# Kernel tuning notes

Measured on AMD Instinct MI355X. Metric: run time of the kernel, lower is better.

Reference implementation:

```python
import jax, jax.numpy as jnp
import numpy as np
import math

B, S, D = 2, 2048, 1024
H = 16
HD = D // H
FFN = 2048
E = 8
TOP_K = 2
CAP_FACTOR = 1.25
EPS = 1e-6
BASE = 10000.0
CAP = max(math.ceil(B * S * TOP_K * CAP_FACTOR / E), 1)  # 1280


def setup_inputs() -> dict:
    key = jax.random.key(0)
    ks = jax.random.split(key, 6)
    sd = 0.02
    return {
        "x": jax.random.normal(ks[0], (B, S, D), jnp.float32),
        "g1": jnp.ones((D,), jnp.float32),
        "w_qkv": jax.random.normal(ks[1], (D, 3 * D), jnp.float32) * sd,
        "w_o": jax.random.normal(ks[2], (D, D), jnp.float32) * sd,
        "g2": jnp.ones((D,), jnp.float32),
        "w_router": jax.random.normal(ks[3], (D, E), jnp.float32) * sd,
        "w1": jax.random.normal(ks[4], (E, D, FFN), jnp.float32) * sd,
        "w2": jax.random.normal(ks[5], (E, FFN, D), jnp.float32) * sd,
    }


def _rmsnorm(x, w):
    rms = jax.lax.rsqrt(jnp.mean(x * x, axis=-1, keepdims=True) + EPS)
    return w * x * rms


def _rope(x, cos, sin):
    # x: [b,h,s,hd]; consecutive pairs (2i, 2i+1) form complex numbers
    xr = x[..., 0::2]
    xi = x[..., 1::2]
    c = cos[None, None]  # [1,1,s,hd/2]
    s_ = sin[None, None]
    out_r = xr * c - xi * s_
    out_i = xr * s_ + xi * c
    return jnp.stack([out_r, out_i], axis=-1).reshape(x.shape)


def _mha(x, w_qkv, w_o):
    b, s, d = x.shape
    qkv = x @ w_qkv
    q, k, v = jnp.split(qkv, 3, axis=-1)
    to_heads = lambda z: z.reshape(b, s, H, HD).transpose(0, 2, 1, 3)
    q, k, v = to_heads(q), to_heads(k), to_heads(v)
    # rotary embedding
    theta = BASE ** (-2.0 * (jnp.arange(HD // 2, dtype=jnp.float32) / HD))
    freqs = jnp.arange(s, dtype=jnp.float32)[:, None] * theta[None, :]  # [s,hd/2]
    cos, sin = jnp.cos(freqs), jnp.sin(freqs)
    q = _rope(q, cos, sin)
    k = _rope(k, cos, sin)
    scores = jnp.einsum('bhqd,bhkd->bhqk', q, k) / jnp.sqrt(jnp.float32(HD))
    causal = jnp.tril(jnp.ones((s, s), dtype=bool))
    scores = jnp.where(causal, scores, -jnp.inf)
    attn = jax.nn.softmax(scores, axis=-1)
    y = jnp.einsum('bhqk,bhkd->bhqd', attn, v)
    y = y.transpose(0, 2, 1, 3).reshape(b, s, d)
    return y @ w_o


def _moe(x, w_router, w1, w2):
    b, s, d = x.shape
    t = b * s
    xf = x.reshape(t, d)
    logits = xf.astype(jnp.float32) @ w_router.astype(jnp.float32)
    probs = jax.nn.softmax(logits, axis=-1)  # [t,E]
    g, eidx = jax.lax.top_k(probs, TOP_K)  # [t,K]
    fg = g.reshape(t * TOP_K)
    fe = eidx.reshape(t * TOP_K)
    tok_of = jnp.arange(t * TOP_K) // TOP_K
    # per-expert masked gates, then capacity-based top-CAP selection
    masked = jnp.where(fe[None, :] == jnp.arange(E)[:, None], fg[None, :], -jnp.inf)  # [E, t*K]
    vals, idx = jax.lax.top_k(masked, CAP)  # [E, CAP]
    valid = jnp.isfinite(vals)
    gates = jnp.where(valid, vals, 0.0)  # dropped/empty slots get zero gate
    tok = tok_of[idx]  # [E, CAP] token ids (arbitrary for invalid slots, gate 0)
    xe = xf[tok]  # [E, CAP, d]
    h = jax.nn.relu(jnp.einsum('ecd,edf->ecf', xe, w1))
    ye = jnp.einsum('ecf,efd->ecd', h, w2) * gates[..., None]
    y = jnp.zeros_like(xf).at[tok.reshape(-1)].add(ye.reshape(-1, d))
    return y.reshape(b, s, d)


def reference(x, g1, w_qkv, w_o, g2, w_router, w1, w2):
    x = x + _mha(_rmsnorm(x, g1), w_qkv, w_o)
    x = x + _moe(_rmsnorm(x, g2), w_router, w1, w2)
    return x
```

## Files before the change

kernel.cpp:

```cpp
#include <hip/hip_runtime.h>
#include <math.h>


#define B_   2
#define S_   2048
#define D_   1024
#define H_   16
#define HD_  64
#define FFN_ 2048
#define E_   8
#define CAP_ 1280
#define T_   (B_*S_)

typedef unsigned short u16;
typedef __attribute__((ext_vector_type(8))) short     short8;
typedef __attribute__((ext_vector_type(8))) _Float16  half8;
typedef __attribute__((ext_vector_type(4))) _Float16  half4;
typedef __attribute__((ext_vector_type(8))) unsigned short ushort8v;
typedef __attribute__((ext_vector_type(4))) float     f32x4;

__device__ __forceinline__ u16 f2bf(float f) {
  unsigned u = __float_as_uint(f);
  return (u16)((u + 0x7fffu + ((u >> 16) & 1u)) >> 16);
}
__device__ __forceinline__ float bf2f(u16 h) {
  return __uint_as_float(((unsigned)h) << 16);
}
__device__ __forceinline__ u16 f2h(float f) {
  _Float16 h = (_Float16)f;
  return __builtin_bit_cast(u16, h);
}
__device__ __forceinline__ float h2f(u16 b) {
  return (float)__builtin_bit_cast(_Float16, b);
}

__device__ __forceinline__ void cstore(float* p, float v) { *p = v; }
__device__ __forceinline__ void cstore(u16* p, float v)   { *p = f2bf(v); }

__device__ __forceinline__ void glds16(const u16* g, u16* l) {
  __builtin_amdgcn_global_load_lds(
      (const __attribute__((address_space(1))) unsigned int*)g,
      (__attribute__((address_space(3))) unsigned int*)l, 16, 0, 0);
}

__global__ void init_k(int* cnt) {
  if (threadIdx.x < 16) cnt[threadIdx.x] = 0;
}

__global__ __launch_bounds__(256) void rmsnorm_k(const float* __restrict__ x,
                                                 const float* __restrict__ g,
                                                 float* __restrict__ of,
                                                 u16*   __restrict__ ob,
                                                 u16*   __restrict__ ohh,
                                                 u16*   __restrict__ ohl) {
  const int t = blockIdx.x, tid = threadIdx.x;
  const float4 xv = ((const float4*)(x + (size_t)t * D_))[tid];
  float ss = xv.x*xv.x + xv.y*xv.y + xv.z*xv.z + xv.w*xv.w;
  #pragma unroll
  for (int off = 32; off; off >>= 1) ss += __shfl_down(ss, off);
  __shared__ float wsum[4];
  if ((tid & 63) == 0) wsum[tid >> 6] = ss;
  __syncthreads();
  const float tot = wsum[0] + wsum[1] + wsum[2] + wsum[3];
  const float rms = 1.0f / sqrtf(tot * (1.0f / D_) + 1e-6f);
  const float4 gv = ((const float4*)g)[tid];
  float4 o;
  o.x = gv.x * xv.x * rms;
  o.y = gv.y * xv.y * rms;
  o.z = gv.z * xv.z * rms;
  o.w = gv.w * xv.w * rms;
  if (of) ((float4*)(of + (size_t)t * D_))[tid] = o;
  if (ob) {
    ushort4 h;
    h.x = f2bf(o.x); h.y = f2bf(o.y); h.z = f2bf(o.z); h.w = f2bf(o.w);
    ((ushort4*)(ob + (size_t)t * D_))[tid] = h;
  }
  if (ohh) {
    ushort4 hh, hl;
    hh.x = f2h(o.x); hl.x = f2h(o.x - h2f(hh.x));
    hh.y = f2h(o.y); hl.y = f2h(o.y - h2f(hh.y));
    hh.z = f2h(o.z); hl.z = f2h(o.z - h2f(hh.z));
    hh.w = f2h(o.w); hl.w = f2h(o.w - h2f(hh.w));
    ((ushort4*)(ohh + (size_t)t * D_))[tid] = hh;
    ((ushort4*)(ohl + (size_t)t * D_))[tid] = hl;
  }
}

template<bool RESID>
__global__ __launch_bounds__(256) void gemm_split(const u16* __restrict__ Ah,
                                                  const u16* __restrict__ Al,
                                                  const u16* __restrict__ Bh,
                                                  const u16* __restrict__ Bl,
                                                  const float* __restrict__ resid,
                                                  float* __restrict__ C,
                                                  int K, int lda, int ldb, int ldc) {
  __shared__ u16 AsH[128 * 32], AsL[128 * 32];
  __shared__ u16 BsH[128 * 32], BsL[128 * 32];
  const int tid = threadIdx.x;
  const int bm = blockIdx.y, bn = blockIdx.x;
  const int lane = tid & 63, wave = tid >> 6;
  const int wy = wave >> 1, wx = wave & 1;
  const int l15 = lane & 15, lq = lane >> 4;
  f32x4 acc[4][4];
  #pragma unroll
  for (int i = 0; i < 4; ++i)
    #pragma unroll
    for (int j = 0; j < 4; ++j)
      #pragma unroll
      for (int r = 0; r < 4; ++r) acc[i][j][r] = 0.0f;
  const int srow = lane >> 2, skc = (lane & 3) * 8;
  size_t ga[2], gb[2];
  int ldsoff[2];
  #pragma unroll
  for (int c = 0; c < 2; ++c) {
    const int q = wave * 2 + c;
    ga[c] = (size_t)(bm * 128 + q * 16 + srow) * lda + skc;
    gb[c] = (size_t)(bn * 128 + q * 16 + srow) * ldb + skc;
    ldsoff[c] = q * 512 + lane * 8;
  }

  for (int kt = 0; kt < K; kt += 32) {
    __syncthreads();
    #pragma unroll
    for (int c = 0; c < 2; ++c) {
      glds16(Ah + ga[c] + kt, &AsH[ldsoff[c]]);
      glds16(Al + ga[c] + kt, &AsL[ldsoff[c]]);
      glds16(Bh + gb[c] + kt, &BsH[ldsoff[c]]);
      glds16(Bl + gb[c] + kt, &BsL[ldsoff[c]]);
    }
    __syncthreads();
    half8 ah[4], al[4], bh[4], bl[4];
    #pragma unroll
    for (int i = 0; i < 4; ++i) {
      const int row = (wy * 64 + i * 16 + l15) * 32 + lq * 8;
      ah[i] = *(const half8*)&AsH[row];
      al[i] = *(const half8*)&AsL[row];
    }
    #pragma unroll
    for (int j = 0; j < 4; ++j) {
      const int row = (wx * 64 + j * 16 + l15) * 32 + lq * 8;
      bh[j] = *(const half8*)&BsH[row];
      bl[j] = *(const half8*)&BsL[row];
    }
    #pragma unroll
    for (int i = 0; i < 4; ++i)
      #pragma unroll
      for (int j = 0; j < 4; ++j) {
        acc[i][j] = __builtin_amdgcn_mfma_f32_16x16x32_f16(ah[i], bh[j], acc[i][j], 0, 0, 0);
        acc[i][j] = __builtin_amdgcn_mfma_f32_16x16x32_f16(ah[i], bl[j], acc[i][j], 0, 0, 0);
        acc[i][j] = __builtin_amdgcn_mfma_f32_16x16x32_f16(al[i], bh[j], acc[i][j], 0, 0, 0);
      }
  }
  #pragma unroll
  for (int i = 0; i < 4; ++i)
    #pragma unroll
    for (int j = 0; j < 4; ++j)
      #pragma unroll
      for (int r = 0; r < 4; ++r) {
        const int row = bm * 128 + wy * 64 + i * 16 + lq * 4 + r;
        const int col = bn * 128 + wx * 64 + j * 16 + l15;
        float v = acc[i][j][r];
        if (RESID) v += resid[(size_t)row * ldc + col];
        C[(size_t)row * ldc + col] = v;
      }
}

__global__ __launch_bounds__(256) void wsplit_t_k(const float* __restrict__ src,
                                                  u16* __restrict__ dh,
                                                  u16* __restrict__ dl,
                                                  int R, int C) {
  __shared__ float tile[32][33];
  const int tid = threadIdx.x;
  const int r0 = blockIdx.y * 32, c0 = blockIdx.x * 32;
  const int tx = tid & 31, ty = tid >> 5;
  #pragma unroll
  for (int i = 0; i < 4; ++i)
    tile[ty + i * 8][tx] = src[(size_t)(r0 + ty + i * 8) * C + c0 + tx];
  __syncthreads();
  #pragma unroll
  for (int i = 0; i < 4; ++i) {
    const float v = tile[tx][ty + i * 8];
    const u16 hh = f2h(v);
    const size_t o = (size_t)(c0 + ty + i * 8) * R + r0 + tx;
    dh[o] = hh;
    dl[o] = f2h(v - h2f(hh));
  }
}

__global__ __launch_bounds__(256) void ropesplit_k(const float* __restrict__ qkv,
                                                   u16* __restrict__ qhi, u16* __restrict__ qlo,
                                                   u16* __restrict__ khi, u16* __restrict__ klo) {
  const int i = blockIdx.x * 256 + threadIdx.x;
  const int j = i & 31;
  const int h = (i >> 5) & 15;
  const int t = i >> 9;
  const int s = t & (S_ - 1);
  const int b = t >> 11;
  const int bh = b * 16 + h;
  const float theta = (float)pow(10000.0, -(double)j / 32.0);
  const float fr = (float)s * theta;
  const float c = cosf(fr), sn = sinf(fr);
  const float2 q = *(const float2*)(qkv + (size_t)t * 3072 + h * 64 + 2 * j);
  const float2 k = *(const float2*)(qkv + (size_t)t * 3072 + 1024 + h * 64 + 2 * j);
  const float q0 = (q.x * c - q.y * sn) * 0.125f;
  const float q1 = (q.x * sn + q.y * c) * 0.125f;
  const float k0 = k.x * c - k.y * sn;
  const float k1 = k.x * sn + k.y * c;
  const size_t o = ((size_t)bh * S_ + s) * 32 + j;
  const u16 qh0 = f2bf(q0), qh1 = f2bf(q1);
  const u16 kh0 = f2bf(k0), kh1 = f2bf(k1);
  ((unsigned*)qhi)[o] = (unsigned)qh0 | ((unsigned)qh1 << 16);
  ((unsigned*)khi)[o] = (unsigned)kh0 | ((unsigned)kh1 << 16);
  const u16 ql0 = f2bf(q0 - bf2f(qh0)), ql1 = f2bf(q1 - bf2f(qh1));
  const u16 kl0 = f2bf(k0 - bf2f(kh0)), kl1 = f2bf(k1 - bf2f(kh1));
  ((unsigned*)qlo)[o] = (unsigned)ql0 | ((unsigned)ql1 << 16);
  ((unsigned*)klo)[o] = (unsigned)kl0 | ((unsigned)kl1 << 16);
}

__global__ __launch_bounds__(256) void vpack_k(const float* __restrict__ qkv,
                                               u16* __restrict__ vpk) {
  const int kt = blockIdx.x, bh = blockIdx.y;
  const int b = bh >> 4, h = bh & 15;
  const int tid = threadIdx.x;
  u16* dst = vpk + (size_t)(bh * 32 + kt) * 8192;
  #pragma unroll
  for (int i = 0; i < 4; ++i) {
    const int g = i * 256 + tid;
    const int lane = g & 63, n = (g >> 6) & 3, kc = g >> 8;
    const int lq = lane >> 4, l15 = lane & 15;
    const int key = kt * 64 + kc * 16 + lq * 4;
    const int d = n * 16 + l15;
    u16 out[8];
    #pragma unroll
    for (int j = 0; j < 4; ++j) {
      const float v = qkv[(size_t)(b * S_ + key + j) * 3072 + 2048 + h * 64 + d];
      const u16 hh = f2h(v);
      out[j] = hh;
      out[4 + j] = f2h(v - h2f(hh));
    }
    *(ushort8v*)(dst + g * 8) = *(ushort8v*)out;
  }
}

__global__ __launch_bounds__(256, 4) void attn_mfma_k(const u16* __restrict__ qhi,
                                                      const u16* __restrict__ qlo,
                                                      const u16* __restrict__ khi,
                                                      const u16* __restrict__ klo,
                                                      const u16* __restrict__ vpk,
                                                      u16* __restrict__ ahh,
                                                      u16* __restrict__ ahl,
                                                      float* __restrict__ PO,
                                                      float* __restrict__ Pm,
                                                      float* __restrict__ Pl2) {
  __shared__ u16 Kh[64 * 68], Kl[64 * 68];
  __shared__ u16 Vp[8192];
  const int tid = threadIdx.x, lane = tid & 63, wave = tid >> 6;
  const int bi = blockIdx.x;
  int qt, k0, k1, chunk;
  bool partial;
  if (bi < 32) {
    qt = 31 - (bi >> 1); chunk = bi & 1;
    const int nk = qt + 1, cut = nk >> 1;
    k0 = chunk ? cut : 0;
    k1 = chunk ? nk : cut;
    partial = true;
  } else {
    qt = 47 - bi; chunk = 0; k0 = 0; k1 = qt + 1; partial = false;
  }
  const int bh = blockIdx.y;
  const int l15 = lane & 15, lq = lane >> 4;
  const size_t hb = (size_t)bh * S_ * 64;
  const int qrow = qt * 64 + wave * 16 + l15;
  short8 qh[2], ql[2];
  qh[0] = *(const short8*)(qhi + hb + (size_t)qrow * 64 + lq * 8);
  qh[1] = *(const short8*)(qhi + hb + (size_t)qrow * 64 + 32 + lq * 8);
  ql[0] = *(const short8*)(qlo + hb + (size_t)qrow * 64 + lq * 8);
  ql[1] = *(const short8*)(qlo + hb + (size_t)qrow * 64 + 32 + lq * 8);
  f32x4 O[4];
  #pragma unroll
  for (int n = 0; n < 4; ++n)
    #pragma unroll
    for (int r = 0; r < 4; ++r) O[n][r] = 0.0f;
  float m_i = -__builtin_inff(), l_i = 0.0f;

  const int sidx0 = tid,       srow0 = sidx0 >> 3, sc80 = (sidx0 & 7) * 8;
  const int sidx1 = 256 + tid, srow1 = sidx1 >> 3, sc81 = (sidx1 & 7) * 8;
  const int vlds = wave * 2048 + lane * 8;
  ushort8v kregH[2], kregL[2], vreg[4];

  auto issue_loads = [&](int kt) {
    const size_t koff0 = hb + (size_t)(kt * 64 + srow0) * 64 + sc80;
    const size_t koff1 = hb + (size_t)(kt * 64 + srow1) * 64 + sc81;
    kregH[0] = *(const ushort8v*)(khi + koff0);
    kregL[0] = *(const ushort8v*)(klo + koff0);
    kregH[1] = *(const ushort8v*)(khi + koff1);
    kregL[1] = *(const ushort8v*)(klo + koff1);
    const u16* vg = vpk + (size_t)(bh * 32 + kt) * 8192 + vlds;
    #pragma unroll
    for (int c = 0; c < 4; ++c)
      vreg[c] = *(const ushort8v*)(vg + c * 512);
  };
  auto write_lds = [&]() {
    *(ushort8v*)&Kh[srow0 * 68 + sc80] = kregH[0];
    *(ushort8v*)&Kl[srow0 * 68 + sc80] = kregL[0];
    *(ushort8v*)&Kh[srow1 * 68 + sc81] = kregH[1];
    *(ushort8v*)&Kl[srow1 * 68 + sc81] = kregL[1];
    #pragma unroll
    for (int c = 0; c < 4; ++c)
      *(ushort8v*)&Vp[vlds + c * 512] = vreg[c];
  };

  issue_loads(k0);
  write_lds();
  __syncthreads();

  for (int kt = k0; kt < k1; ++kt) {
    const bool pf = (kt + 1 < k1);
    if (pf) issue_loads(kt + 1);
    f32x4 sc[4];
    #pragma unroll
    for (int kc = 0; kc < 4; ++kc)
      #pragma unroll
      for (int r = 0; r < 4; ++r) sc[kc][r] = 0.0f;
    __builtin_amdgcn_s_setprio(1);
    #pragma unroll
    for (int kc = 0; kc < 4; ++kc) {
      const int krow = (kc * 16 + l15) * 68 + lq * 8;
      const short8 kb0 = *(const short8*)&Kh[krow];
      const short8 kb1 = *(const short8*)&Kh[krow + 32];
      const short8 kl0 = *(const short8*)&Kl[krow];
      const short8 kl1 = *(const short8*)&Kl[krow + 32];
      sc[kc] = __builtin_amdgcn_mfma_f32_16x16x32_bf16(kb0, qh[0], sc[kc], 0, 0, 0);
      sc[kc] = __builtin_amdgcn_mfma_f32_16x16x32_bf16(kb1, qh[1], sc[kc], 0, 0, 0);
      sc[kc] = __builtin_amdgcn_mfma_f32_16x16x32_bf16(kb0, ql[0], sc[kc], 0, 0, 0);
      sc[kc] = __builtin_amdgcn_mfma_f32_16x16x32_bf16(kb1, ql[1], sc[kc], 0, 0, 0);
      sc[kc] = __builtin_amdgcn_mfma_f32_16x16x32_bf16(kl0, qh[0], sc[kc], 0, 0, 0);
      sc[kc] = __builtin_amdgcn_mfma_f32_16x16x32_bf16(kl1, qh[1], sc[kc], 0, 0, 0);
    }
    __builtin_amdgcn_s_setprio(0);
    if (kt == qt) {
      #pragma unroll
      for (int kc = 0; kc < 4; ++kc)
        #pragma unroll
        for (int r = 0; r < 4; ++r)
          if (kc * 16 + lq * 4 + r > wave * 16 + l15) sc[kc][r] = -__builtin_inff();
    }
    float mx = -__builtin_inff();
    #pragma unroll
    for (int kc = 0; kc < 4; ++kc)
      #pragma unroll
      for (int r = 0; r < 4; ++r) mx = fmaxf(mx, sc[kc][r]);
    mx = fmaxf(mx, __shfl_xor(mx, 16));
    mx = fmaxf(mx, __shfl_xor(mx, 32));
    const float mn = fmaxf(m_i, mx);
    const float alpha = __expf(m_i - mn);
    m_i = mn;
    f32x4 p[4];
    float rs = 0.0f;
    #pragma unroll
    for (int kc = 0; kc < 4; ++kc)
      #pragma unroll
      for (int r = 0; r < 4; ++r) { p[kc][r] = __expf(sc[kc][r] - m_i); rs += p[kc][r]; }
    rs += __shfl_xor(rs, 16);
    rs += __shfl_xor(rs, 32);
    l_i = l_i * alpha + rs;
    #pragma unroll
    for (int r = 0; r < 4; ++r) {
      const float alr = __shfl(alpha, lq * 4 + r);
      #pragma unroll
      for (int n = 0; n < 4; ++n) O[n][r] *= alr;
    }
    half4 ph[4], pl[4];
    #pragma unroll
    for (int kc = 0; kc < 4; ++kc)
      #pragma unroll
      for (int r = 0; r < 4; ++r) {
        const _Float16 hi = (_Float16)p[kc][r];
        ph[kc][r] = hi;
        pl[kc][r] = (_Float16)(p[kc][r] - (float)hi);
      }
    __builtin_amdgcn_s_setprio(1);
    #pragma unroll
    for (int n = 0; n < 4; ++n)
      #pragma unroll
      for (int kc = 0; kc < 4; ++kc) {
        const int g = ((kc * 4 + n) * 64 + lane) * 8;
        const half4 vh = *(const half4*)&Vp[g];
        const half4 vl = *(const half4*)&Vp[g + 4];
        O[n] = __builtin_amdgcn_mfma_f32_16x16x16f16(ph[kc], vh, O[n], 0, 0, 0);
        O[n] = __builtin_amdgcn_mfma_f32_16x16x16f16(ph[kc], vl, O[n], 0, 0, 0);
        O[n] = __builtin_amdgcn_mfma_f32_16x16x16f16(pl[kc], vh, O[n], 0, 0, 0);
      }
    __builtin_amdgcn_s_setprio(0);
    __syncthreads();
    if (pf) write_lds();
    __syncthreads();
  }
  const int b = bh >> 4, h = bh & 15;
  if (!partial) {
    #pragma unroll
    for (int r = 0; r < 4; ++r) {
      const float lr = __shfl(l_i, lq * 4 + r);
      const float inv = 1.0f / lr;
      const int row = qt * 64 + wave * 16 + lq * 4 + r;
      const size_t base = (size_t)(b * S_ + row) * D_ + h * 64 + l15;
      #pragma unroll
      for (int n = 0; n < 4; ++n) {
        const float o = O[n][r] * inv;
        const u16 hh = f2h(o);
        ahh[base + n * 16] = hh;
        ahl[base + n * 16] = f2h(o - h2f(hh));
      }
    }
  } else {
    #pragma unroll
    for (int r = 0; r < 4; ++r) {
      const int prow = qt * 64 + wave * 16 + lq * 4 + r - 1024;
      const size_t idx = (size_t)(chunk * 32 + bh) * 1024 + prow;
      float* po = PO + idx * 64;
      #pragma unroll
      for (int n = 0; n < 4; ++n) po[n * 16 + l15] = O[n][r];
    }
    if (lq == 0) {
      const int prow = qt * 64 + wave * 16 + l15 - 1024;
      const size_t idx = (size_t)(chunk * 32 + bh) * 1024 + prow;
      Pm[idx] = m_i; Pl2[idx] = l_i;
    }
  }
}

__global__ __launch_bounds__(256) void attn_combine_k(const float* __restrict__ PO,
                                                      const float* __restrict__ Pm,
                                                      const float* __restrict__ Pl2,
                                                      u16* __restrict__ ahh,
                                                      u16* __restrict__ ahl) {
  const int tid = threadIdx.x;
  const int bh = blockIdx.y, b = bh >> 4, h = bh & 15;
  const int prow = blockIdx.x * 64 + (tid >> 2);
  const int d0 = (tid & 3) * 16;
  const size_t i0 = (size_t)bh * 1024 + prow;
  const size_t i1 = (size_t)(32 + bh) * 1024 + prow;
  const float m0 = Pm[i0], m1 = Pm[i1];
  const float M = fmaxf(m0, m1);
  const float w0 = __expf(m0 - M), w1 = __expf(m1 - M);
  const float inv = 1.0f / (w0 * Pl2[i0] + w1 * Pl2[i1]);
  const int row = 1024 + prow;
  const size_t ob = (size_t)(b * S_ + row) * D_ + h * 64 + d0;
  #pragma unroll
  for (int q4 = 0; q4 < 4; ++q4) {
    const float4 o0 = *(const float4*)(PO + i0 * 64 + d0 + q4 * 4);
    const float4 o1 = *(const float4*)(PO + i1 * 64 + d0 + q4 * 4);
    float v[4];
    v[0] = (w0 * o0.x + w1 * o1.x) * inv;
    v[1] = (w0 * o0.y + w1 * o1.y) * inv;
    v[2] = (w0 * o0.z + w1 * o1.z) * inv;
    v[3] = (w0 * o0.w + w1 * o1.w) * inv;
    ushort4 hh, hl;
    u16* ph = (u16*)&hh;
    u16* pl = (u16*)&hl;
    #pragma unroll
    for (int z = 0; z < 4; ++z) {
      ph[z] = f2h(v[z]);
      pl[z] = f2h(v[z] - h2f(ph[z]));
    }
    *(ushort4*)(ahh + ob + q4 * 4) = hh;
    *(ushort4*)(ahl + ob + q4 * 4) = hl;
  }
}

__global__ __launch_bounds__(256) void router_k(const float* __restrict__ y2,
                                                const float* __restrict__ wr,
                                                int*   __restrict__ cnt,
                                                int*   __restrict__ tok_e,
                                                float* __restrict__ tok_g,
                                                int*   __restrict__ tok_p,
                                                int*   __restrict__ etok) {
  const int wave = threadIdx.x >> 6, lane = threadIdx.x & 63;
  const int t = blockIdx.x * 4 + wave;
  const float* xr = y2 + (size_t)t * D_;
  float acc[8];
  #pragma unroll
  for (int e = 0; e < 8; ++e) acc[e] = 0.0f;
  for (int c = 0; c < 16; ++c) {
    const float xv = xr[c * 64 + lane];
    const float* w = wr + (size_t)(c * 64 + lane) * 8;
    #pragma unroll
    for (int e = 0; e < 8; ++e) acc[e] = fmaf(xv, w[e], acc[e]);
  }
  #pragma unroll
  for (int off = 32; off; off >>= 1)
    #pragma unroll
    for (int e = 0; e < 8; ++e) acc[e] += __shfl_down(acc[e], off);
  if (lane == 0) {
    float mx = acc[0];
    #pragma unroll
    for (int e = 1; e < 8; ++e) mx = fmaxf(mx, acc[e]);
    float ex[8], sum = 0.0f;
    #pragma unroll
    for (int e = 0; e < 8; ++e) { ex[e] = expf(acc[e] - mx); sum += ex[e]; }
    int e1 = 0;
    #pragma unroll
    for (int e = 1; e < 8; ++e) if (acc[e] > acc[e1]) e1 = e;
    int e2 = (e1 == 0) ? 1 : 0;
    #pragma unroll
    for (int e = 0; e < 8; ++e) if (e != e1 && acc[e] > acc[e2]) e2 = e;
    const float g1v = ex[e1] / sum, g2v = ex[e2] / sum;
    int p1 = atomicAdd(&cnt[e1], 1);
    int p2 = atomicAdd(&cnt[e2], 1);
    if (p1 < CAP_) etok[e1 * CAP_ + p1] = t; else p1 = -1;
    if (p2 < CAP_) etok[e2 * CAP_ + p2] = t; else p2 = -1;
    tok_e[2*t] = e1;   tok_e[2*t+1] = e2;
    tok_g[2*t] = g1v;  tok_g[2*t+1] = g2v;
    tok_p[2*t] = p1;   tok_p[2*t+1] = p2;
  }
}

__global__ __launch_bounds__(256) void gather_k(const u16* __restrict__ y2b,
                                                const int* __restrict__ etok,
                                                const int* __restrict__ cnt,
                                                u16* __restrict__ xe) {
  const int e = blockIdx.y, pos = blockIdx.x, tid = threadIdx.x;
  const int n = min(cnt[e], CAP_);
  ushort4* dst = (ushort4*)(xe + (size_t)(e * CAP_ + pos) * D_) + tid;
  if (pos < n) {
    const int t = etok[e * CAP_ + pos];
    *dst = ((const ushort4*)(y2b + (size_t)t * D_))[tid];
  } else {
    *dst = make_ushort4(0, 0, 0, 0);
  }
}

template<typename OT, bool RELU>
__global__ __launch_bounds__(256) void gemm_bt(const u16* __restrict__ A,
                                               const u16* __restrict__ Bt,
                                               OT* __restrict__ C,
                                               int M, int N, int K,
                                               int lda, int ldb, int ldc,
                                               long sAz, long sBz, long sCz) {
  __shared__ u16 As[128 * 32];
  __shared__ u16 Bs[128 * 32];
  const int tid = threadIdx.x;
  A  += (size_t)blockIdx.z * sAz;
  Bt += (size_t)blockIdx.z * sBz;
  C  += (size_t)blockIdx.z * sCz;
  const int bm = blockIdx.y, bn = blockIdx.x;
  const int lane = tid & 63, wave = tid >> 6;
  const int wy = wave >> 1, wx = wave & 1;
  const int l15 = lane & 15, lq = lane >> 4;
  f32x4 acc[4][4];
  #pragma unroll
  for (int i = 0; i < 4; ++i)
    #pragma unroll
    for (int j = 0; j < 4; ++j)
      #pragma unroll
      for (int r = 0; r < 4; ++r) acc[i][j][r] = 0.0f;
  const int srow = lane >> 2, skc = (lane & 3) * 8;
  size_t ga[2], gb[2];
  int ldsoff[2];
  #pragma unroll
  for (int c = 0; c < 2; ++c) {
    const int q = wave * 2 + c;
    ga[c] = (size_t)(bm * 128 + q * 16 + srow) * lda + skc;
    gb[c] = (size_t)(bn * 128 + q * 16 + srow) * ldb + skc;
    ldsoff[c] = q * 512 + lane * 8;
  }

  for (int kt = 0; kt < K; kt += 32) {
    __syncthreads();
    #pragma unroll
    for (int c = 0; c < 2; ++c) {
      glds16(A  + ga[c] + kt, &As[ldsoff[c]]);
      glds16(Bt + gb[c] + kt, &Bs[ldsoff[c]]);
    }
    __syncthreads();
    short8 a[4], b[4];
    #pragma unroll
    for (int i = 0; i < 4; ++i)
      a[i] = *(const short8*)&As[(wy * 64 + i * 16 + l15) * 32 + lq * 8];
    #pragma unroll
    for (int j = 0; j < 4; ++j)
      b[j] = *(const short8*)&Bs[(wx * 64 + j * 16 + l15) * 32 + lq * 8];
    #pragma unroll
    for (int i = 0; i < 4; ++i)
      #pragma unroll
      for (int j = 0; j < 4; ++j)
        acc[i][j] = __builtin_amdgcn_mfma_f32_16x16x32_bf16(a[i], b[j], acc[i][j], 0, 0, 0);
  }
  #pragma unroll
  for (int i = 0; i < 4; ++i)
    #pragma unroll
    for (int j = 0; j < 4; ++j)
      #pragma unroll
      for (int r = 0; r < 4; ++r) {
        const int row = bm * 128 + wy * 64 + i * 16 + lq * 4 + r;
        const int col = bn * 128 + wx * 64 + j * 16 + l15;
        float v = acc[i][j][r];
        if (RELU) v = fmaxf(v, 0.0f);
        cstore(C + (size_t)row * ldc + col, v);
      }
}

__global__ __launch_bounds__(256) void transpose_bf_k(const float* __restrict__ src,
                                                      u16* __restrict__ dst,
                                                      int R, int C) {
  __shared__ float tile[32][33];
  const int tid = threadIdx.x;
  const size_t zoff = (size_t)blockIdx.z * R * C;
  const int r0 = blockIdx.y * 32, c0 = blockIdx.x * 32;
  const int tx = tid & 31, ty = tid >> 5;
  #pragma unroll
  for (int i = 0; i < 4; ++i)
    tile[ty + i * 8][tx] = src[zoff + (size_t)(r0 + ty + i * 8) * C + c0 + tx];
  __syncthreads();
  #pragma unroll
  for (int i = 0; i < 4; ++i)
    dst[zoff + (size_t)(c0 + ty + i * 8) * R + r0 + tx] = f2bf(tile[tx][ty + i * 8]);
}

__global__ __launch_bounds__(256) void combine_k(const float* __restrict__ x2,
                                                 const float* __restrict__ ye,
                                                 const int*   __restrict__ tok_e,
                                                 const float* __restrict__ tok_g,
                                                 const int*   __restrict__ tok_p,
                                                 float* __restrict__ out) {
  const int t = blockIdx.x, tid = threadIdx.x;
  float4 v = ((const float4*)(x2 + (size_t)t * D_))[tid];
  #pragma unroll
  for (int r = 0; r < 2; ++r) {
    const int p = tok_p[2 * t + r];
    if (p >= 0) {
      const int e = tok_e[2 * t + r];
      const float g = tok_g[2 * t + r];
      const float4 y = ((const float4*)(ye + (size_t)(e * CAP_ + p) * D_))[tid];
      v.x = fmaf(g, y.x, v.x);
      v.y = fmaf(g, y.y, v.y);
      v.z = fmaf(g, y.z, v.z);
      v.w = fmaf(g, y.w, v.w);
    }
  }
  ((float4*)(out + (size_t)t * D_))[tid] = v;
}

extern "C" void kernel_launch(void* const* d_in, const int* in_sizes, int n_in,
                              void* d_out, int out_size, void* d_ws, size_t ws_size,
                              hipStream_t stream) {
  const float* x    = (const float*)d_in[0];
  const float* g1   = (const float*)d_in[1];
  const float* wqkv = (const float*)d_in[2];
  const float* wo   = (const float*)d_in[3];
  const float* g2   = (const float*)d_in[4];
  const float* wr   = (const float*)d_in[5];
  const float* w1   = (const float*)d_in[6];
  const float* w2   = (const float*)d_in[7];
  float* out = (float*)d_out;
  char* ws = (char*)d_ws;
  const size_t MB = 1ull << 20;

  u16*   y1hh  = (u16*)  (ws + 0);
  u16*   y1hl  = (u16*)  (ws + 8 * MB);
  u16*   ahh   = (u16*)  (ws + 16 * MB);
  u16*   ahl   = (u16*)  (ws + 24 * MB);
  u16*   hbf   = (u16*)  (ws + 0);
  float* qkv   = (float*)(ws + 40 * MB);
  float* PO    = (float*)(ws + 40 * MB);
  float* Pm    = (float*)(ws + 58 * MB);
  float* Pl2   = (float*)(ws + 59 * MB);
  u16*   xe    = (u16*)  (ws + 40 * MB);
  float* x2    = (float*)(ws + 88 * MB);
  float* y2    = (float*)(ws + 104 * MB);
  u16*   y2b   = (u16*)  (ws + 120 * MB);
  u16*   w1t   = (u16*)  (ws + 128 * MB);
  u16*   w2t   = (u16*)  (ws + 160 * MB);
  float* ye    = (float*)(ws + 192 * MB);
  u16*   wqh   = (u16*)  (ws + 192 * MB);
  u16*   wql   = (u16*)  (ws + 198 * MB);
  u16*   khi   = (u16*)  (ws + 192 * MB);
  u16*   klo   = (u16*)  (ws + 200 * MB);
  u16*   vpk   = (u16*)  (ws + 208 * MB);
  u16*   woh   = (u16*)  (ws + 224 * MB);
  u16*   wol   = (u16*)  (ws + 226 * MB);
  int*   cnt   = (int*)  (ws + 232 * MB);
  int*   tok_e = cnt + 16;
  float* tok_g = (float*)(tok_e + 2 * T_);
  int*   tok_p = (int*)  (tok_g + 2 * T_);
  int*   etok  = tok_p + 2 * T_;

  init_k<<<1, 64, 0, stream>>>(cnt);
  transpose_bf_k<<<dim3(FFN_/32, D_/32, E_), 256, 0, stream>>>(w1, w1t, D_, FFN_);
  transpose_bf_k<<<dim3(D_/32, FFN_/32, E_), 256, 0, stream>>>(w2, w2t, FFN_, D_);
  wsplit_t_k<<<dim3(3*D_/32, D_/32), 256, 0, stream>>>(wqkv, wqh, wql, D_, 3*D_);
  wsplit_t_k<<<dim3(D_/32, D_/32), 256, 0, stream>>>(wo, woh, wol, D_, D_);

  rmsnorm_k<<<T_, 256, 0, stream>>>(x, g1, (float*)nullptr, (u16*)nullptr, y1hh, y1hl);
  gemm_split<false><<<dim3(3 * D_ / 128, T_ / 128), 256, 0, stream>>>(
      y1hh, y1hl, wqh, wql, nullptr, qkv, D_, D_, D_, 3 * D_);
  ropesplit_k<<<T_ * H_ * 32 / 256, 256, 0, stream>>>(qkv, y1hh, y1hl, khi, klo);
  vpack_k<<<dim3(S_ / 64, B_ * H_), 256, 0, stream>>>(qkv, vpk);
  attn_mfma_k<<<dim3(48, B_ * H_), 256, 0, stream>>>(
      y1hh, y1hl, khi, klo, vpk, ahh, ahl, PO, Pm, Pl2);
  attn_combine_k<<<dim3(16, B_ * H_), 256, 0, stream>>>(PO, Pm, Pl2, ahh, ahl);
  gemm_split<true><<<dim3(D_ / 128, T_ / 128), 256, 0, stream>>>(
      ahh, ahl, woh, wol, x, x2, D_, D_, D_, D_);
  rmsnorm_k<<<T_, 256, 0, stream>>>(x2, g2, y2, y2b, (u16*)nullptr, (u16*)nullptr);
  router_k<<<T_ / 4, 256, 0, stream>>>(y2, wr, cnt, tok_e, tok_g, tok_p, etok);
  gather_k<<<dim3(CAP_, E_), 256, 0, stream>>>(y2b, etok, cnt, xe);
  gemm_bt<u16, true><<<dim3(FFN_/128, CAP_/128, E_), 256, 0, stream>>>(
      xe, w1t, hbf, CAP_, FFN_, D_, D_, D_, FFN_,
      (long)CAP_ * D_, (long)FFN_ * D_, (long)CAP_ * FFN_);
  gemm_bt<float, false><<<dim3(D_/128, CAP_/128, E_), 256, 0, stream>>>(
      hbf, w2t, ye, CAP_, D_, FFN_, FFN_, FFN_, D_,
      (long)CAP_ * FFN_, (long)D_ * FFN_, (long)CAP_ * D_);
  combine_k<<<T_, 256, 0, stream>>>(x2, ye, tok_e, tok_g, tok_p, out);
}
```

Measured before the change: 745.1 us.

## Split attention KV into 8-tile chunks, swizzle K LDS, double-buffer MoE GEMM

Causal attention work is now split into fixed chunks of 8 key tiles, giving 80 blocks per head instead of 48 for finer load balance. Partial results are stored in 72 slots per head, and the combine kernel merges 2 to 4 partials per query tile. The K tiles in LDS move from padded rows to an XOR swizzle to avoid bank conflicts. The batched MoE GEMM gets double-buffered LDS so the next K-slice loads while MFMAs run, at the cost of extra LDS and more partial-result traffic.

```diff
diff --git a/kernel.cpp b/kernel.cpp
--- a/kernel.cpp
+++ b/kernel.cpp
@@ -11,6 +11,7 @@
 #define E_   8
 #define CAP_ 1280
 #define T_   (B_*S_)
+#define NSLOT_ 72
 
 typedef unsigned short u16;
 typedef __attribute__((ext_vector_type(8))) short     short8;
@@ -252,21 +253,24 @@
                                                       float* __restrict__ PO,
                                                       float* __restrict__ Pm,
                                                       float* __restrict__ Pl2) {
-  __shared__ u16 Kh[64 * 68], Kl[64 * 68];
+  __shared__ u16 Kh[64 * 64], Kl[64 * 64];
   __shared__ u16 Vp[8192];
   const int tid = threadIdx.x, lane = tid & 63, wave = tid >> 6;
   const int bi = blockIdx.x;
-  int qt, k0, k1, chunk;
-  bool partial;
-  if (bi < 32) {
-    qt = 31 - (bi >> 1); chunk = bi & 1;
-    const int nk = qt + 1, cut = nk >> 1;
-    k0 = chunk ? cut : 0;
-    k1 = chunk ? nk : cut;
-    partial = true;
-  } else {
-    qt = 47 - bi; chunk = 0; k0 = 0; k1 = qt + 1; partial = false;
-  }
+  int qt, j;
+  if (bi < 32)      { qt = 24 + (bi >> 2);        j = bi & 3; }
+  else if (bi < 56) { qt = 16 + (bi - 32) / 3;    j = (bi - 32) % 3; }
+  else if (bi < 72) { qt = 8 + ((bi - 56) >> 1);  j = (bi - 56) & 1; }
+  else              { qt = bi - 72;               j = 0; }
+  const int k0 = j * 8;
+  const int k1_ = k0 + 8, nk = qt + 1;
+  const int k1 = (k1_ < nk) ? k1_ : nk;
+  const bool partial = (qt >= 8);
+  int slot = 0;
+  if (partial)
+    slot = (qt < 16) ? (qt - 8) * 2 + j
+         : (qt < 24) ? 16 + (qt - 16) * 3 + j
+                     : 40 + (qt - 24) * 4 + j;
   const int bh = blockIdx.y;
   const int l15 = lane & 15, lq = lane >> 4;
   const size_t hb = (size_t)bh * S_ * 64;
@@ -283,8 +287,10 @@
     for (int r = 0; r < 4; ++r) O[n][r] = 0.0f;
   float m_i = -__builtin_inff(), l_i = 0.0f;
 
-  const int sidx0 = tid,       srow0 = sidx0 >> 3, sc80 = (sidx0 & 7) * 8;
-  const int sidx1 = 256 + tid, srow1 = sidx1 >> 3, sc81 = (sidx1 & 7) * 8;
+  const int srow0 = tid >> 3,         sc80 = (tid & 7) * 8;
+  const int srow1 = (256 + tid) >> 3, sc81 = sc80;
+  const int swz0 = srow0 * 64 + (sc80 ^ ((srow0 & 7) << 3));
+  const int swz1 = srow1 * 64 + (sc81 ^ ((srow1 & 7) << 3));
   const int vlds = wave * 2048 + lane * 8;
   ushort8v kregH[2], kregL[2], vreg[4];
 
@@ -301,10 +307,10 @@
       vreg[c] = *(const ushort8v*)(vg + c * 512);
   };
   auto write_lds = [&]() {
-    *(ushort8v*)&Kh[srow0 * 68 + sc80] = kregH[0];
-    *(ushort8v*)&Kl[srow0 * 68 + sc80] = kregL[0];
-    *(ushort8v*)&Kh[srow1 * 68 + sc81] = kregH[1];
-    *(ushort8v*)&Kl[srow1 * 68 + sc81] = kregL[1];
+    *(ushort8v*)&Kh[swz0] = kregH[0];
+    *(ushort8v*)&Kl[swz0] = kregL[0];
+    *(ushort8v*)&Kh[swz1] = kregH[1];
+    *(ushort8v*)&Kl[swz1] = kregL[1];
     #pragma unroll
     for (int c = 0; c < 4; ++c)
       *(ushort8v*)&Vp[vlds + c * 512] = vreg[c];
@@ -325,11 +331,12 @@
     __builtin_amdgcn_s_setprio(1);
     #pragma unroll
     for (int kc = 0; kc < 4; ++kc) {
-      const int krow = (kc * 16 + l15) * 68 + lq * 8;
-      const short8 kb0 = *(const short8*)&Kh[krow];
-      const short8 kb1 = *(const short8*)&Kh[krow + 32];
-      const short8 kl0 = *(const short8*)&Kl[krow];
-      const short8 kl1 = *(const short8*)&Kl[krow + 32];
+      const int row = kc * 16 + l15;
+      const int x = (row & 7) << 3;
+      const short8 kb0 = *(const short8*)&Kh[row * 64 + ((lq * 8) ^ x)];
+      const short8 kb1 = *(const short8*)&Kh[row * 64 + ((32 + lq * 8) ^ x)];
+      const short8 kl0 = *(const short8*)&Kl[row * 64 + ((lq * 8) ^ x)];
+      const short8 kl1 = *(const short8*)&Kl[row * 64 + ((32 + lq * 8) ^ x)];
       sc[kc] = __builtin_amdgcn_mfma_f32_16x16x32_bf16(kb0, qh[0], sc[kc], 0, 0, 0);
       sc[kc] = __builtin_amdgcn_mfma_f32_16x16x32_bf16(kb1, qh[1], sc[kc], 0, 0, 0);
       sc[kc] = __builtin_amdgcn_mfma_f32_16x16x32_bf16(kb0, ql[0], sc[kc], 0, 0, 0);
@@ -415,15 +422,15 @@
   } else {
     #pragma unroll
     for (int r = 0; r < 4; ++r) {
-      const int prow = qt * 64 + wave * 16 + lq * 4 + r - 1024;
-      const size_t idx = (size_t)(chunk * 32 + bh) * 1024 + prow;
+      const int lr = wave * 16 + lq * 4 + r;
+      const size_t idx = ((size_t)bh * NSLOT_ + slot) * 64 + lr;
       float* po = PO + idx * 64;
       #pragma unroll
       for (int n = 0; n < 4; ++n) po[n * 16 + l15] = O[n][r];
     }
     if (lq == 0) {
-      const int prow = qt * 64 + wave * 16 + l15 - 1024;
-      const size_t idx = (size_t)(chunk * 32 + bh) * 1024 + prow;
+      const int lr = wave * 16 + l15;
+      const size_t idx = ((size_t)bh * NSLOT_ + slot) * 64 + lr;
       Pm[idx] = m_i; Pl2[idx] = l_i;
     }
   }
@@ -435,33 +442,47 @@
                                                       u16* __restrict__ ahh,
                                                       u16* __restrict__ ahl) {
   const int tid = threadIdx.x;
+  const int qt = 8 + blockIdx.x;
   const int bh = blockIdx.y, b = bh >> 4, h = bh & 15;
-  const int prow = blockIdx.x * 64 + (tid >> 2);
+  const int Cq  = (qt < 16) ? 2 : (qt < 24 ? 3 : 4);
+  const int off = (qt < 16) ? (qt - 8) * 2
+                : (qt < 24) ? 16 + (qt - 16) * 3
+                            : 40 + (qt - 24) * 4;
+  const int lr = tid >> 2;
   const int d0 = (tid & 3) * 16;
-  const size_t i0 = (size_t)bh * 1024 + prow;
-  const size_t i1 = (size_t)(32 + bh) * 1024 + prow;
-  const float m0 = Pm[i0], m1 = Pm[i1];
-  const float M = fmaxf(m0, m1);
-  const float w0 = __expf(m0 - M), w1 = __expf(m1 - M);
-  const float inv = 1.0f / (w0 * Pl2[i0] + w1 * Pl2[i1]);
-  const int row = 1024 + prow;
+  float m[4], w[4];
+  float M = -__builtin_inff();
+  for (int c = 0; c < Cq; ++c) {
+    m[c] = Pm[((size_t)bh * NSLOT_ + off + c) * 64 + lr];
+    M = fmaxf(M, m[c]);
+  }
+  float L = 0.0f;
+  for (int c = 0; c < Cq; ++c) {
+    w[c] = __expf(m[c] - M);
+    L += w[c] * Pl2[((size_t)bh * NSLOT_ + off + c) * 64 + lr];
+  }
+  const float inv = 1.0f / L;
+  const int row = qt * 64 + lr;
   const size_t ob = (size_t)(b * S_ + row) * D_ + h * 64 + d0;
   #pragma unroll
   for (int q4 = 0; q4 < 4; ++q4) {
-    const float4 o0 = *(const float4*)(PO + i0 * 64 + d0 + q4 * 4);
-    const float4 o1 = *(const float4*)(PO + i1 * 64 + d0 + q4 * 4);
-    float v[4];
-    v[0] = (w0 * o0.x + w1 * o1.x) * inv;
-    v[1] = (w0 * o0.y + w1 * o1.y) * inv;
-    v[2] = (w0 * o0.z + w1 * o1.z) * inv;
-    v[3] = (w0 * o0.w + w1 * o1.w) * inv;
+    float v[4] = {0.0f, 0.0f, 0.0f, 0.0f};
+    for (int c = 0; c < Cq; ++c) {
+      const float4 o = *(const float4*)(PO +
+          (((size_t)bh * NSLOT_ + off + c) * 64 + lr) * 64 + d0 + q4 * 4);
+      v[0] = fmaf(w[c], o.x, v[0]);
+      v[1] = fmaf(w[c], o.y, v[1]);
+      v[2] = fmaf(w[c], o.z, v[2]);
+      v[3] = fmaf(w[c], o.w, v[3]);
+    }
     ushort4 hh, hl;
     u16* ph = (u16*)&hh;
     u16* pl = (u16*)&hl;
     #pragma unroll
     for (int z = 0; z < 4; ++z) {
-      ph[z] = f2h(v[z]);
-      pl[z] = f2h(v[z] - h2f(ph[z]));
+      const float vn = v[z] * inv;
+      ph[z] = f2h(vn);
+      pl[z] = f2h(vn - h2f(ph[z]));
     }
     *(ushort4*)(ahh + ob + q4 * 4) = hh;
     *(ushort4*)(ahl + ob + q4 * 4) = hl;
@@ -537,8 +558,8 @@
                                                int M, int N, int K,
                                                int lda, int ldb, int ldc,
                                                long sAz, long sBz, long sCz) {
-  __shared__ u16 As[128 * 32];
-  __shared__ u16 Bs[128 * 32];
+  __shared__ u16 As[2][128 * 32];
+  __shared__ u16 Bs[2][128 * 32];
   const int tid = threadIdx.x;
   A  += (size_t)blockIdx.z * sAz;
   Bt += (size_t)blockIdx.z * sBz;
@@ -564,27 +585,33 @@
     gb[c] = (size_t)(bn * 128 + q * 16 + srow) * ldb + skc;
     ldsoff[c] = q * 512 + lane * 8;
   }
-
+  auto stage = [&](int buf, int kt) {
+    #pragma unroll
+    for (int c = 0; c < 2; ++c) {
+      glds16(A  + ga[c] + kt, &As[buf][ldsoff[c]]);
+      glds16(Bt + gb[c] + kt, &Bs[buf][ldsoff[c]]);
+    }
+  };
+
+  stage(0, 0);
+  __syncthreads();
+  int cur = 0;
   for (int kt = 0; kt < K; kt += 32) {
-    __syncthreads();
-    #pragma unroll
-    for (int c = 0; c < 2; ++c) {
-      glds16(A  + ga[c] + kt, &As[ldsoff[c]]);
-      glds16(Bt + gb[c] + kt, &Bs[ldsoff[c]]);
-    }
-    __syncthreads();
+    if (kt + 32 < K) stage(cur ^ 1, kt + 32);
     short8 a[4], b[4];
     #pragma unroll
     for (int i = 0; i < 4; ++i)
-      a[i] = *(const short8*)&As[(wy * 64 + i * 16 + l15) * 32 + lq * 8];
+      a[i] = *(const short8*)&As[cur][(wy * 64 + i * 16 + l15) * 32 + lq * 8];
     #pragma unroll
     for (int j = 0; j < 4; ++j)
-      b[j] = *(const short8*)&Bs[(wx * 64 + j * 16 + l15) * 32 + lq * 8];
+      b[j] = *(const short8*)&Bs[cur][(wx * 64 + j * 16 + l15) * 32 + lq * 8];
     #pragma unroll
     for (int i = 0; i < 4; ++i)
       #pragma unroll
       for (int j = 0; j < 4; ++j)
         acc[i][j] = __builtin_amdgcn_mfma_f32_16x16x32_bf16(a[i], b[j], acc[i][j], 0, 0, 0);
+    __syncthreads();
+    cur ^= 1;
   }
   #pragma unroll
   for (int i = 0; i < 4; ++i)
@@ -663,8 +690,8 @@
   u16*   hbf   = (u16*)  (ws + 0);
   float* qkv   = (float*)(ws + 40 * MB);
   float* PO    = (float*)(ws + 40 * MB);
-  float* Pm    = (float*)(ws + 58 * MB);
-  float* Pl2   = (float*)(ws + 59 * MB);
+  float* Pm    = (float*)(ws + 78 * MB);
+  float* Pl2   = (float*)(ws + 79 * MB);
   u16*   xe    = (u16*)  (ws + 40 * MB);
   float* x2    = (float*)(ws + 88 * MB);
   float* y2    = (float*)(ws + 104 * MB);
@@ -696,9 +723,9 @@
       y1hh, y1hl, wqh, wql, nullptr, qkv, D_, D_, D_, 3 * D_);
   ropesplit_k<<<T_ * H_ * 32 / 256, 256, 0, stream>>>(qkv, y1hh, y1hl, khi, klo);
   vpack_k<<<dim3(S_ / 64, B_ * H_), 256, 0, stream>>>(qkv, vpk);
-  attn_mfma_k<<<dim3(48, B_ * H_), 256, 0, stream>>>(
+  attn_mfma_k<<<dim3(80, B_ * H_), 256, 0, stream>>>(
       y1hh, y1hl, khi, klo, vpk, ahh, ahl, PO, Pm, Pl2);
-  attn_combine_k<<<dim3(16, B_ * H_), 256, 0, stream>>>(PO, Pm, Pl2, ahh, ahl);
+  attn_combine_k<<<dim3(24, B_ * H_), 256, 0, stream>>>(PO, Pm, Pl2, ahh, ahl);
   gemm_split<true><<<dim3(D_ / 128, T_ / 128), 256, 0, stream>>>(
       ahh, ahl, woh, wol, x, x2, D_, D_, D_, D_);
   rmsnorm_k<<<T_, 256, 0, stream>>>(x2, g2, y2, y2b, (u16*)nullptr, (u16*)nullptr);
```

Result: faster. 720.8 us (-3.3%).
